# Kernel optimization log

Measured on AMD Instinct MI355X. Metric: run time of the kernel, lower is better.

Reference implementation:

```python
import jax, jax.numpy as jnp
import numpy as np

CATS = [1000, 1000, 2000]
NDS = len(CATS)
TOT = sum(CATS)          # total_cats = 4000
N = TOT + NDS            # 4003 source (label) nodes
U = 2048                 # num_unify_class
NFEAT = 256
F = 256                  # nfeat_out
OUT_FEAT = 512           # output_feat_dim
ADJ_FEAT = 256           # adj_feat_dim
SINKHORN_ITERS = 20


def setup_inputs() -> dict:
    key = jax.random.key(0)
    ks = jax.random.split(key, 16)

    def rn(k, shape, s):
        return jax.random.normal(k, shape, dtype=jnp.float32) * s

    return {
        "datasets_node_features": jax.random.normal(ks[0], (TOT, NFEAT), dtype=jnp.float32),
        "unlable_node_features": rn(ks[1], (NDS, NFEAT), 0.02),  # trunc_normal_(std=0.02)
        "adj_matrix": jax.random.uniform(ks[2], (N, U), dtype=jnp.float32),  # torch.rand init
        "W_before": rn(ks[3], (NFEAT, F), 0.05), "b_before": jnp.zeros((F,), jnp.float32),
        "gc1_W": rn(ks[4], (F, F), 0.05), "gc1_b": jnp.zeros((F,), jnp.float32),
        "gc2_W": rn(ks[5], (F, F), 0.05), "gc2_b": jnp.zeros((F,), jnp.float32),
        "gc3_W": rn(ks[6], (F, F), 0.05), "gc3_b": jnp.zeros((F,), jnp.float32),
        "W1": rn(ks[7], (F, OUT_FEAT), 0.05), "b1": jnp.zeros((OUT_FEAT,), jnp.float32),
        "W2": rn(ks[8], (OUT_FEAT, ADJ_FEAT), 0.05), "b2": jnp.zeros((ADJ_FEAT,), jnp.float32),
    }


def _log_optimal_transport(scores, iters):
    # log-space Sinkhorn with uniform marginals 1/(m+n), then rescale by (m+n)
    m, n = scores.shape
    norm = -jnp.log(jnp.asarray(m + n, scores.dtype))
    log_mu = jnp.full((m,), norm, scores.dtype)
    log_nu = jnp.full((n,), norm, scores.dtype)

    def body(carry, _):
        u, v = carry
        u = log_mu - jax.nn.logsumexp(scores + v[None, :], axis=1)
        v = log_nu - jax.nn.logsumexp(scores + u[:, None], axis=0)
        return (u, v), None

    (u, v), _ = jax.lax.scan(body, (jnp.zeros_like(log_mu), jnp.zeros_like(log_nu)),
                             None, length=iters)
    return scores + u[:, None] + v[None, :] - norm


def reference(datasets_node_features, unlable_node_features, adj_matrix,
              W_before, b_before, gc1_W, gc1_b, gc2_W, gc2_b, gc3_W, gc3_b,
              W1, b1, W2, b2):
    # node features: dataset class nodes + per-dataset 'unlabeled' nodes -> [N, NFEAT]
    feats = jnp.concatenate([datasets_node_features, unlable_node_features], axis=0)
    x = jax.nn.relu(feats @ W_before + b_before)  # [N, F]

    # learnable adjacency normalized via differentiable Sinkhorn OT  [N, U]
    A = jnp.exp(_log_optimal_transport(adj_matrix, SINKHORN_ITERS))

    # bipartite message passing: full graph adj has zero diagonal blocks,
    # so spmm(adj, h) splits into A @ h_u (into label nodes) and A.T @ h_n (into unify nodes).
    hn = x                 # [N, F] label-node features
    hu = A.T @ x           # [U, F] initial unify-node features via aggregation

    def gcn(hn, hu, W, b):
        # GraphConvolution: spmm(adj, h @ W) + b ; GCN wrapper: tanh(out + h)
        new_n = jnp.tanh(A @ (hu @ W) + b + hn)
        new_u = jnp.tanh(A.T @ (hn @ W) + b + hu)
        return new_n, new_u

    hn, hu = gcn(hn, hu, gc1_W, gc1_b)
    hn, hu = gcn(hn, hu, gc2_W, gc2_b)
    hn, hu = gcn(hn, hu, gc3_W, gc3_b)

    # output head on unify nodes: linear1 -> relu -> linear2  [U, ADJ_FEAT]
    out = jax.nn.relu(hu @ W1 + b1) @ W2 + b2
    return out
```

## Files before the change

kernel.cpp:

```cpp
#include <hip/hip_runtime.h>
#include <hip/hip_fp16.h>
#include <math.h>

#define NN 4003
#define UU 2048
#define KP 4032
#define N4P 4004
#define NORMC (-8.7079796f)

using bf16x8 = __attribute__((ext_vector_type(8))) short;
using f32x4  = __attribute__((ext_vector_type(4))) float;

#define GLL16(g, l) __builtin_amdgcn_global_load_lds( \
    (const __attribute__((address_space(1))) unsigned*)(g), \
    (__attribute__((address_space(3))) unsigned*)(l), 16, 0, 0)

__device__ __forceinline__ ushort f2bf(float x) {
    unsigned u = __builtin_bit_cast(unsigned, x);
    u += 0x7fff + ((u >> 16) & 1);
    return (ushort)(u >> 16);
}
__device__ __forceinline__ float bf2f(ushort h) {
    unsigned u = ((unsigned)h) << 16;
    return __builtin_bit_cast(float, u);
}
__device__ __forceinline__ void bfsplit(float x, ushort& hi, ushort& lo) {
    hi = f2bf(x);
    lo = f2bf(x - bf2f(hi));
}
__device__ __forceinline__ float h2f(ushort h) {
    return __half2float(__ushort_as_half(h));
}

__global__ void concat_bf(const float* __restrict__ a, const float* __restrict__ b,
                          ushort* __restrict__ fh, ushort* __restrict__ fl) {
    int i = blockIdx.x * 256 + threadIdx.x;
    const int tot4 = NN * 256 / 4;
    if (i >= tot4) return;
    float4 v = (i < 256000) ? ((const float4*)a)[i] : ((const float4*)b)[i - 256000];
    ushort4 hv, lv;
    bfsplit(v.x, hv.x, lv.x); bfsplit(v.y, hv.y, lv.y);
    bfsplit(v.z, hv.z, lv.z); bfsplit(v.w, hv.w, lv.w);
    *(ushort4*)(fh + ((size_t)i << 2)) = hv;
    *(ushort4*)(fl + ((size_t)i << 2)) = lv;
}

__global__ void convW(const float* __restrict__ W, ushort* __restrict__ Th,
                      ushort* __restrict__ Tl, int K, int Nw) {
    __shared__ float tile[32][33];
    int bx = blockIdx.x, by = blockIdx.y;
    int tx = threadIdx.x;
    for (int r = threadIdx.y; r < 32; r += 8)
        tile[r][tx] = W[(size_t)(by * 32 + r) * Nw + bx * 32 + tx];
    __syncthreads();
    for (int r = threadIdx.y; r < 32; r += 8) {
        int n = bx * 32 + r, k = by * 32 + tx;
        ushort hi, lo; bfsplit(tile[tx][r], hi, lo);
        Th[(size_t)n * K + k] = hi;
        Tl[(size_t)n * K + k] = lo;
    }
}

__global__ void conv_both(const float* __restrict__ in, ushort* __restrict__ Sh,
                          ushort* __restrict__ STh) {
    __shared__ float tile[32][33];
    int x = blockIdx.x * 32 + threadIdx.x;
    int y0 = blockIdx.y * 32;
    for (int r = threadIdx.y; r < 32; r += 8) {
        int y = y0 + r;
        float vv = (y < NN) ? in[(size_t)y * UU + x] : 0.0f;
        tile[r][threadIdx.x] = vv;
        if (y < NN)
            Sh[(size_t)y * UU + x] = __half_as_ushort(__float2half(vv));
    }
    __syncthreads();
    int oc = y0 + threadIdx.x;
    for (int r = threadIdx.y; r < 32; r += 8) {
        int orow = blockIdx.x * 32 + r;
        STh[(size_t)orow * KP + oc] = __half_as_ushort(__float2half(tile[threadIdx.x][r]));
    }
}

__global__ void init_uext(float* __restrict__ u_ext) {
    int i = threadIdx.x;
    if (i < KP - NN) u_ext[NN + i] = -1e30f;
}

__global__ __launch_bounds__(256) void lse2h(const ushort* __restrict__ Sh, int lda,
                                             const float* __restrict__ addv,
                                             float* __restrict__ outv, int C, int R) {
    int r0 = blockIdx.x * 2, r1 = r0 + 1;
    bool has1 = (r1 < R);
    const ushort* rowa = Sh + (size_t)r0 * lda;
    const ushort* rowb = Sh + (size_t)(has1 ? r1 : r0) * lda;
    const float4* a4 = (const float4*)addv;
    float m0 = -INFINITY, s0 = 0.0f, m1 = -INFINITY, s1 = 0.0f;
    int C4 = C >> 2;
    for (int j = threadIdx.x; j < C4; j += 256) {
        float4 av = a4[j];
        ushort4 pa = *(const ushort4*)(rowa + (j << 2));
        ushort4 pb = *(const ushort4*)(rowb + (j << 2));
        float a0 = h2f(pa.x) + av.x, a1 = h2f(pa.y) + av.y;
        float a2 = h2f(pa.z) + av.z, a3 = h2f(pa.w) + av.w;
        float b0 = h2f(pb.x) + av.x, b1 = h2f(pb.y) + av.y;
        float b2 = h2f(pb.z) + av.z, b3 = h2f(pb.w) + av.w;
        float mxa = fmaxf(fmaxf(a0, a1), fmaxf(a2, a3));
        float nm0 = fmaxf(m0, mxa);
        s0 = s0 * __expf(m0 - nm0) + __expf(a0 - nm0) + __expf(a1 - nm0)
                                   + __expf(a2 - nm0) + __expf(a3 - nm0);
        m0 = nm0;
        float mxb = fmaxf(fmaxf(b0, b1), fmaxf(b2, b3));
        float nm1 = fmaxf(m1, mxb);
        s1 = s1 * __expf(m1 - nm1) + __expf(b0 - nm1) + __expf(b1 - nm1)
                                   + __expf(b2 - nm1) + __expf(b3 - nm1);
        m1 = nm1;
    }
    int rem = C & 3;
    if ((int)threadIdx.x < rem) {
        int j = (C4 << 2) + threadIdx.x;
        float av = addv[j];
        float xa = h2f(rowa[j]) + av;
        float nm0 = fmaxf(m0, xa);
        s0 = s0 * __expf(m0 - nm0) + __expf(xa - nm0);
        m0 = nm0;
        float xb = h2f(rowb[j]) + av;
        float nm1 = fmaxf(m1, xb);
        s1 = s1 * __expf(m1 - nm1) + __expf(xb - nm1);
        m1 = nm1;
    }
    #pragma unroll
    for (int off = 1; off < 64; off <<= 1) {
        float om = __shfl_xor(m0, off, 64), os = __shfl_xor(s0, off, 64);
        float nm = fmaxf(m0, om);
        s0 = s0 * __expf(m0 - nm) + os * __expf(om - nm);
        m0 = nm;
        om = __shfl_xor(m1, off, 64); os = __shfl_xor(s1, off, 64);
        nm = fmaxf(m1, om);
        s1 = s1 * __expf(m1 - nm) + os * __expf(om - nm);
        m1 = nm;
    }
    __shared__ float sm[8], ss[8];
    int w = threadIdx.x >> 6;
    if ((threadIdx.x & 63) == 0) { sm[w] = m0; ss[w] = s0; sm[4 + w] = m1; ss[4 + w] = s1; }
    __syncthreads();
    if (threadIdx.x < 2) {
        int b = threadIdx.x * 4;
        float m = sm[b], s = ss[b];
        #pragma unroll
        for (int i = 1; i < 4; ++i) {
            float om = sm[b + i], os = ss[b + i];
            float nm = fmaxf(m, om);
            s = s * __expf(m - nm) + os * __expf(om - nm);
            m = nm;
        }
        int r = r0 + threadIdx.x;
        if (threadIdx.x == 0 || has1) outv[r] = NORMC - (m + __logf(s));
    }
}

__device__ __forceinline__ void exp_row8h(const ushort* __restrict__ Sh,
        const float* __restrict__ rowadd, const float* __restrict__ coladd,
        int lda, int M, int gm, int kbase, uint4& hiv, uint4& lov) {
    ushort h[8], l[8];
    if (gm < M) {
        float ra = rowadd[gm] - NORMC;
        const ushort* rp = Sh + (size_t)gm * lda + kbase;
        ushort4 q0 = *(const ushort4*)rp;
        ushort4 q1 = *(const ushort4*)(rp + 4);
        float4 ca = *(const float4*)(coladd + kbase);
        float4 cb = *(const float4*)(coladd + kbase + 4);
        float vv[8] = {h2f(q0.x) + ca.x, h2f(q0.y) + ca.y, h2f(q0.z) + ca.z, h2f(q0.w) + ca.w,
                       h2f(q1.x) + cb.x, h2f(q1.y) + cb.y, h2f(q1.z) + cb.z, h2f(q1.w) + cb.w};
        #pragma unroll
        for (int e = 0; e < 8; ++e) {
            float av = __expf(vv[e] + ra);
            bfsplit(av, h[e], l[e]);
        }
    } else {
        #pragma unroll
        for (int e = 0; e < 8; ++e) { h[e] = 0; l[e] = 0; }
    }
    hiv.x = (unsigned)h[0] | ((unsigned)h[1] << 16);
    hiv.y = (unsigned)h[2] | ((unsigned)h[3] << 16);
    hiv.z = (unsigned)h[4] | ((unsigned)h[5] << 16);
    hiv.w = (unsigned)h[6] | ((unsigned)h[7] << 16);
    lov.x = (unsigned)l[0] | ((unsigned)l[1] << 16);
    lov.y = (unsigned)l[2] | ((unsigned)l[3] << 16);
    lov.z = (unsigned)l[4] | ((unsigned)l[5] << 16);
    lov.w = (unsigned)l[6] | ((unsigned)l[7] << 16);
}

__global__ __launch_bounds__(512) __attribute__((amdgpu_waves_per_eu(2, 4)))
void gemm_bigN(
        const ushort* __restrict__ Sh, const float* __restrict__ rowadd,
        const float* __restrict__ coladd, int lda,
        const ushort* __restrict__ Bh, const ushort* __restrict__ Bl, int ldb,
        float* __restrict__ P, int M, int K, int Kc) {
    __shared__ __align__(16) ushort SM[2 * 64 * 64 + 2 * 256 * 64];
    ushort* As0 = SM;
    ushort* As1 = SM + 4096;
    ushort* Bs0 = SM + 8192;
    ushort* Bs1 = SM + 8192 + 16384;
    const int tid = threadIdx.x;
    const int bm = blockIdx.x << 6;
    const int lane = tid & 63;
    const int wv = tid >> 6;
    const int wr = (wv >> 2) << 5;
    const int wc = (wv & 3) << 6;
    const int kb = blockIdx.y * Kc;
    int ke = kb + Kc; if (ke > K) ke = K;
    const int arow = tid >> 3, ak8 = (tid & 7) << 3;
    const int as = ((arow << 6) + ak8) ^ ((arow & 7) << 3);
    const int brow_base = wv << 5;
    f32x4 acc[2][4] = {};
    for (int k0 = kb; k0 < ke; k0 += 64) {
        uint4 ah, al;
        exp_row8h(Sh, rowadd, coladd, lda, M, bm + arow, k0 + ak8, ah, al);
        __syncthreads();
        #pragma unroll
        for (int t = 0; t < 4; ++t) {
            int rb2 = brow_base + (t << 3);
            int row = rb2 + (lane >> 3);
            int kksrc = (((lane & 7) ^ (row & 7)) << 3);
            size_t go = (size_t)row * ldb + k0 + kksrc;
            GLL16(Bh + go, &Bs0[rb2 << 6]);
            GLL16(Bl + go, &Bs1[rb2 << 6]);
        }
        *(uint4*)&As0[as] = ah;
        *(uint4*)&As1[as] = al;
        __syncthreads();
        #pragma unroll
        for (int ks = 0; ks < 2; ++ks) {
            int kq = (ks << 5) + ((lane >> 4) << 3);
            bf16x8 fah[2], fal[2], fbh[4], fbl[4];
            #pragma unroll
            for (int f = 0; f < 2; ++f) {
                int rr = wr + (f << 4) + (lane & 15);
                int ia = ((rr << 6) + kq) ^ ((rr & 7) << 3);
                fah[f] = *(const bf16x8*)&As0[ia];
                fal[f] = *(const bf16x8*)&As1[ia];
            }
            #pragma unroll
            for (int g = 0; g < 4; ++g) {
                int cc = wc + (g << 4) + (lane & 15);
                int ib = ((cc << 6) + kq) ^ ((cc & 7) << 3);
                fbh[g] = *(const bf16x8*)&Bs0[ib];
                fbl[g] = *(const bf16x8*)&Bs1[ib];
            }
            #pragma unroll
            for (int i = 0; i < 2; ++i)
                #pragma unroll
                for (int j = 0; j < 4; ++j) {
                    acc[i][j] = __builtin_amdgcn_mfma_f32_16x16x32_bf16(fah[i], fbh[j], acc[i][j], 0, 0, 0);
                    acc[i][j] = __builtin_amdgcn_mfma_f32_16x16x32_bf16(fah[i], fbl[j], acc[i][j], 0, 0, 0);
                    acc[i][j] = __builtin_amdgcn_mfma_f32_16x16x32_bf16(fal[i], fbh[j], acc[i][j], 0, 0, 0);
                }
        }
    }
    __syncthreads();
    float* LF = (float*)SM;
    #pragma unroll
    for (int i = 0; i < 2; ++i) {
        int row0 = wr + (i << 4) + ((lane >> 4) << 2);
        #pragma unroll
        for (int j = 0; j < 4; ++j) {
            int col = wc + (j << 4) + (lane & 15);
            #pragma unroll
            for (int r = 0; r < 4; ++r)
                LF[(row0 + r) * 256 + col] = acc[i][j][r];
        }
    }
    __syncthreads();
    float* Pp = P + (size_t)blockIdx.y * ((size_t)M * 256);
    #pragma unroll
    for (int it = 0; it < 8; ++it) {
        int idx = tid + (it << 9);
        int row = idx >> 6, c4 = (idx & 63) << 2;
        if (bm + row < M)
            *(float4*)(Pp + (size_t)(bm + row) * 256 + c4) = *(const float4*)&LF[row * 256 + c4];
    }
}

__global__ __launch_bounds__(256) __attribute__((amdgpu_waves_per_eu(4, 8)))
void gemm_ks(
        const ushort* __restrict__ Ah, const ushort* __restrict__ Al, int lda,
        const ushort* __restrict__ Bh, const ushort* __restrict__ Bl, int ldb, int Nb,
        float* __restrict__ P, int M, int Nplane, int K, int Kc) {
    __shared__ __align__(16) ushort SM[4 * 64 * 64];
    ushort* As0 = SM;
    ushort* As1 = SM + 4096;
    ushort* Bs0 = SM + 8192;
    ushort* Bs1 = SM + 12288;
    const int tid = threadIdx.x;
    const int bm = blockIdx.y << 6, bn = blockIdx.x << 6;
    const int lane = tid & 63;
    const int wv = tid >> 6;
    const int wm = (wv >> 1) << 5, wn = (wv & 1) << 5;
    const int kb = blockIdx.z * Kc;
    int ke = kb + Kc; if (ke > K) ke = K;
    const int rb = wv << 4;
    f32x4 acc[2][2] = {};
    for (int k0 = kb; k0 < ke; k0 += 64) {
        __syncthreads();
        #pragma unroll
        for (int t = 0; t < 2; ++t) {
            int rb2 = rb + (t << 3);
            int row = rb2 + (lane >> 3);
            int kksrc = (((lane & 7) ^ (row & 7)) << 3);
            int ga = bm + row; ga = (ga < M) ? ga : (M - 1);
            int gb = bn + row; gb = (gb < Nb) ? gb : (Nb - 1);
            size_t goa = (size_t)ga * lda + k0 + kksrc;
            size_t gob = (size_t)gb * ldb + k0 + kksrc;
            GLL16(Ah + goa, &As0[rb2 << 6]);
            GLL16(Al + goa, &As1[rb2 << 6]);
            GLL16(Bh + gob, &Bs0[rb2 << 6]);
            GLL16(Bl + gob, &Bs1[rb2 << 6]);
        }
        __syncthreads();
        #pragma unroll
        for (int ks = 0; ks < 2; ++ks) {
            int kbq = (ks << 5) + ((lane >> 4) << 3);
            bf16x8 fah[2], fal[2], fbh[2], fbl[2];
            #pragma unroll
            for (int f = 0; f < 2; ++f) {
                int rr = wm + (f << 4) + (lane & 15);
                int ia = ((rr << 6) + kbq) ^ ((rr & 7) << 3);
                fah[f] = *(const bf16x8*)&As0[ia];
                fal[f] = *(const bf16x8*)&As1[ia];
                int cc = wn + (f << 4) + (lane & 15);
                int ib = ((cc << 6) + kbq) ^ ((cc & 7) << 3);
                fbh[f] = *(const bf16x8*)&Bs0[ib];
                fbl[f] = *(const bf16x8*)&Bs1[ib];
            }
            #pragma unroll
            for (int i = 0; i < 2; ++i)
                #pragma unroll
                for (int j = 0; j < 2; ++j) {
                    acc[i][j] = __builtin_amdgcn_mfma_f32_16x16x32_bf16(fah[i], fbh[j], acc[i][j], 0, 0, 0);
                    acc[i][j] = __builtin_amdgcn_mfma_f32_16x16x32_bf16(fah[i], fbl[j], acc[i][j], 0, 0, 0);
                    acc[i][j] = __builtin_amdgcn_mfma_f32_16x16x32_bf16(fal[i], fbh[j], acc[i][j], 0, 0, 0);
                }
        }
    }
    __syncthreads();
    float* LF = (float*)SM;
    #pragma unroll
    for (int i = 0; i < 2; ++i) {
        int row0 = wm + (i << 4) + ((lane >> 4) << 2);
        #pragma unroll
        for (int j = 0; j < 2; ++j) {
            int col = wn + (j << 4) + (lane & 15);
            #pragma unroll
            for (int r = 0; r < 4; ++r)
                LF[(row0 + r) * 64 + col] = acc[i][j][r];
        }
    }
    __syncthreads();
    float* Pp = P + (size_t)blockIdx.z * ((size_t)M * Nplane);
    #pragma unroll
    for (int it = 0; it < 4; ++it) {
        int idx = tid + (it << 8);
        int row = idx >> 4, c4 = (idx & 15) << 2;
        if (bm + row < M && bn + c4 < Nplane)
            *(float4*)(Pp + (size_t)(bm + row) * Nplane + bn + c4) = *(const float4*)&LF[row * 64 + c4];
    }
}

template<int ACT, int BIAS, int RES, int OUTK>
__global__ __launch_bounds__(256) void reduce_ks(
        const float* __restrict__ P, int zg,
        const float* __restrict__ bias,
        const ushort* __restrict__ Rh, const ushort* __restrict__ Rl,
        float* __restrict__ Cf, ushort* __restrict__ Ch, ushort* __restrict__ Cl,
        int M, int N4, int ldo) {
    int t = blockIdx.x * 256 + threadIdx.x;
    int n4w = N4 >> 2;
    int tot = M * n4w;
    if (t >= tot) return;
    int m = t / n4w;
    int n = (t - m * n4w) << 2;
    size_t pstr = (size_t)M * N4;
    const float* base = P + (size_t)m * N4 + n;
    float4 a = *(const float4*)base;
    for (int z = 1; z < zg; ++z) {
        float4 b = *(const float4*)(base + (size_t)z * pstr);
        a.x += b.x; a.y += b.y; a.z += b.z; a.w += b.w;
    }
    if (BIAS == 1) {
        float4 bv = *(const float4*)(bias + n);
        a.x += bv.x; a.y += bv.y; a.z += bv.z; a.w += bv.w;
    }
    if (BIAS == 2) {
        float s = bias[m];
        a.x += s; a.y += s; a.z += s; a.w += s;
    }
    if (RES) {
        size_t ro = (size_t)m * ldo + n;
        ushort4 rh = *(const ushort4*)(Rh + ro);
        ushort4 rl = *(const ushort4*)(Rl + ro);
        a.x += bf2f(rh.x) + bf2f(rl.x); a.y += bf2f(rh.y) + bf2f(rl.y);
        a.z += bf2f(rh.z) + bf2f(rl.z); a.w += bf2f(rh.w) + bf2f(rl.w);
    }
    if (ACT == 1) {
        a.x = fmaxf(a.x, 0.f); a.y = fmaxf(a.y, 0.f);
        a.z = fmaxf(a.z, 0.f); a.w = fmaxf(a.w, 0.f);
    }
    if (ACT == 2) {
        a.x = tanhf(a.x); a.y = tanhf(a.y); a.z = tanhf(a.z); a.w = tanhf(a.w);
    }
    size_t co = (size_t)m * ldo + n;
    if (OUTK == 0) {
        *(float4*)(Cf + co) = a;
    } else {
        ushort4 hv, lv;
        bfsplit(a.x, hv.x, lv.x); bfsplit(a.y, hv.y, lv.y);
        bfsplit(a.z, hv.z, lv.z); bfsplit(a.w, hv.w, lv.w);
        *(ushort4*)(Ch + co) = hv;
        *(ushort4*)(Cl + co) = lv;
    }
}

static inline int rgrid(int M, int N4) { return (M * (N4 >> 2) + 255) / 256; }

extern "C" void kernel_launch(void* const* d_in, const int* in_sizes, int n_in,
                              void* d_out, int out_size, void* d_ws, size_t ws_size,
                              hipStream_t stream) {
    const float* dsf = (const float*)d_in[0];
    const float* unl = (const float*)d_in[1];
    const float* S   = (const float*)d_in[2];
    const float* Wb  = (const float*)d_in[3];
    const float* bb  = (const float*)d_in[4];
    const float* gcW[3] = {(const float*)d_in[5], (const float*)d_in[7], (const float*)d_in[9]};
    const float* gcb[3] = {(const float*)d_in[6], (const float*)d_in[8], (const float*)d_in[10]};
    const float* W1 = (const float*)d_in[11];
    const float* b1 = (const float*)d_in[12];
    const float* W2 = (const float*)d_in[13];
    const float* b2 = (const float*)d_in[14];
    float* out = (float*)d_out;

    char* p = (char*)d_ws;
    ushort* Shm = (ushort*)p; p += (size_t)NN * UU * 2;
    ushort* STh = (ushort*)p; p += (size_t)UU * KP * 2;
    float* P    = (float*)p;  p += (size_t)8 * NN * 256 * 4;
    ushort* fh = (ushort*)p; ushort* fl = fh + (size_t)NN * 256; p += (size_t)NN * 256 * 4;
    ushort* xh = (ushort*)p; ushort* xl = xh + (size_t)NN * 256; p += (size_t)NN * 256 * 4;
    ushort* xTh = (ushort*)p; ushort* xTl = xTh + (size_t)256 * KP; p += (size_t)256 * KP * 4;
    ushort* huh = (ushort*)p; ushort* hul = huh + (size_t)UU * 256; p += (size_t)UU * 256 * 4;
    ushort* tuTh = (ushort*)p; ushort* tuTl = tuTh + (size_t)256 * UU; p += (size_t)256 * UU * 4;
    ushort* tnTh = (ushort*)p; ushort* tnTl = tnTh + (size_t)256 * KP; p += (size_t)256 * KP * 4;
    float* u_ext = (float*)p; p += KP * 4;
    float* v     = (float*)p; p += UU * 4;
    ushort* WbTh = (ushort*)p; ushort* WbTl = WbTh + 256 * 256; p += 256 * 256 * 4;
    ushort* gWh[3]; ushort* gWl[3];
    for (int l = 0; l < 3; ++l) { gWh[l] = (ushort*)p; gWl[l] = gWh[l] + 256 * 256; p += 256 * 256 * 4; }
    ushort* W1Th = (ushort*)p; ushort* W1Tl = W1Th + 512 * 256; p += 512 * 256 * 4;
    ushort* W2Th = (ushort*)p; ushort* W2Tl = W2Th + 256 * 512; p += 256 * 512 * 4;
    ushort* h1h = xh; ushort* h1l = h1h + (size_t)UU * 512;
    (void)ws_size;

    concat_bf<<<dim3(1001), dim3(256), 0, stream>>>(dsf, unl, fh, fl);
    convW<<<dim3(8, 8),  dim3(32, 8), 0, stream>>>(Wb, WbTh, WbTl, 256, 256);
    for (int l = 0; l < 3; ++l)
        convW<<<dim3(8, 8), dim3(32, 8), 0, stream>>>(gcW[l], gWh[l], gWl[l], 256, 256);
    convW<<<dim3(16, 8), dim3(32, 8), 0, stream>>>(W1, W1Th, W1Tl, 256, 512);
    convW<<<dim3(8, 16), dim3(32, 8), 0, stream>>>(W2, W2Th, W2Tl, 512, 256);
    init_uext<<<dim3(1), dim3(64), 0, stream>>>(u_ext);
    conv_both<<<dim3(64, 126), dim3(32, 8), 0, stream>>>(S, Shm, STh);
    hipMemsetAsync(v, 0, UU * sizeof(float), stream);

    gemm_ks<<<dim3(4, 63, 4), 256, 0, stream>>>(
        fh, fl, 256, WbTh, WbTl, 256, 256, P, NN, 256, 256, 64);
    reduce_ks<1,1,0,1><<<rgrid(NN,256), 256, 0, stream>>>(
        P, 4, bb, nullptr, nullptr, nullptr, xh, xl, NN, 256, 256);
    gemm_ks<<<dim3(63, 4, 4), 256, 0, stream>>>(
        WbTh, WbTl, 256, fh, fl, 256, NN, P, 256, N4P, 256, 64);
    reduce_ks<1,2,0,1><<<rgrid(256,N4P), 256, 0, stream>>>(
        P, 4, bb, nullptr, nullptr, nullptr, xTh, xTl, 256, N4P, KP);

    for (int it = 0; it < 20; ++it) {
        lse2h<<<dim3((NN + 1) / 2), dim3(256), 0, stream>>>(Shm, UU, v, u_ext, UU, NN);
        lse2h<<<dim3(UU / 2),       dim3(256), 0, stream>>>(STh, KP, u_ext, v, NN, UU);
    }

    gemm_bigN<<<dim3(32, 8), 512, 0, stream>>>(
        STh, v, u_ext, KP, xTh, xTl, KP, P, UU, KP, 512);
    reduce_ks<0,0,0,1><<<rgrid(UU,256), 256, 0, stream>>>(
        P, 8, nullptr, nullptr, nullptr, nullptr, huh, hul, UU, 256, 256);

    for (int l = 0; l < 3; ++l) {
        const ushort* hnh = (l == 0) ? xh : fh;
        const ushort* hnl = (l == 0) ? xl : fl;
        if (l < 2) {
            gemm_ks<<<dim3(32, 4, 4), 256, 0, stream>>>(
                gWh[l], gWl[l], 256, huh, hul, 256, UU, P, 256, UU, 256, 64);
            reduce_ks<0,0,0,1><<<rgrid(256,UU), 256, 0, stream>>>(
                P, 4, nullptr, nullptr, nullptr, nullptr, tuTh, tuTl, 256, UU, UU);
        }
        gemm_ks<<<dim3(63, 4, 4), 256, 0, stream>>>(
            gWh[l], gWl[l], 256, hnh, hnl, 256, NN, P, 256, N4P, 256, 64);
        reduce_ks<0,0,0,1><<<rgrid(256,N4P), 256, 0, stream>>>(
            P, 4, nullptr, nullptr, nullptr, nullptr, tnTh, tnTl, 256, N4P, KP);
        if (l < 2) {
            gemm_bigN<<<dim3(63, 8), 512, 0, stream>>>(
                Shm, u_ext, v, UU, tuTh, tuTl, UU, P, NN, UU, 256);
            reduce_ks<2,1,1,1><<<rgrid(NN,256), 256, 0, stream>>>(
                P, 8, gcb[l], hnh, hnl, nullptr, fh, fl, NN, 256, 256);
        }
        gemm_bigN<<<dim3(32, 8), 512, 0, stream>>>(
            STh, v, u_ext, KP, tnTh, tnTl, KP, P, UU, KP, 512);
        reduce_ks<2,1,1,1><<<rgrid(UU,256), 256, 0, stream>>>(
            P, 8, gcb[l], huh, hul, nullptr, huh, hul, UU, 256, 256);
    }

    gemm_ks<<<dim3(8, 32, 4), 256, 0, stream>>>(
        huh, hul, 256, W1Th, W1Tl, 256, 512, P, UU, 512, 256, 64);
    reduce_ks<1,1,0,1><<<rgrid(UU,512), 256, 0, stream>>>(
        P, 4, b1, nullptr, nullptr, nullptr, h1h, h1l, UU, 512, 512);
    gemm_ks<<<dim3(4, 32, 8), 256, 0, stream>>>(
        h1h, h1l, 512, W2Th, W2Tl, 512, 256, P, UU, 256, 512, 64);
    reduce_ks<0,1,0,0><<<rgrid(UU,256), 256, 0, stream>>>(
        P, 8, b2, nullptr, nullptr, out, nullptr, nullptr, UU, 256, 256);
}
```

Measured before the change: 587.5 us.

## Merge setup kernels, process four rows per Sinkhorn block, halve GEMM split-K

Several small setup launches are merged into single kernels: weight conversions go through one convW_all grid, and the u_ext/v initialisation is folded into concat_bf. The Sinkhorn logsumexp kernel now handles four rows per block instead of two, which reuses each addv load across more rows and halves the block count. The split-K factors of most GEMMs drop from 4 (or 8) to 2 (or 4, or 6), with larger K chunks, so less partial-sum traffic goes through reduce_ks. This costs some parallelism on the smaller GEMMs and adds register pressure in the LSE kernel.

```diff
diff --git a/kernel.cpp b/kernel.cpp
--- a/kernel.cpp
+++ b/kernel.cpp
@@ -33,22 +33,48 @@
 }
 
 __global__ void concat_bf(const float* __restrict__ a, const float* __restrict__ b,
-                          ushort* __restrict__ fh, ushort* __restrict__ fl) {
-    int i = blockIdx.x * 256 + threadIdx.x;
+                          ushort* __restrict__ fh, ushort* __restrict__ fl,
+                          float* __restrict__ u_ext, float* __restrict__ v) {
+    int bid = blockIdx.x;
+    if (bid >= 1001) {
+        if (bid < 1003) {
+            int t = (bid - 1001) * 256 + threadIdx.x;
+            if (t < 512) ((float4*)v)[t] = (float4){0.f, 0.f, 0.f, 0.f};
+        } else {
+            if ((int)threadIdx.x < KP - NN) u_ext[NN + threadIdx.x] = -1e30f;
+        }
+        return;
+    }
+    int i = bid * 256 + threadIdx.x;
     const int tot4 = NN * 256 / 4;
     if (i >= tot4) return;
-    float4 v = (i < 256000) ? ((const float4*)a)[i] : ((const float4*)b)[i - 256000];
+    float4 vv = (i < 256000) ? ((const float4*)a)[i] : ((const float4*)b)[i - 256000];
     ushort4 hv, lv;
-    bfsplit(v.x, hv.x, lv.x); bfsplit(v.y, hv.y, lv.y);
-    bfsplit(v.z, hv.z, lv.z); bfsplit(v.w, hv.w, lv.w);
+    bfsplit(vv.x, hv.x, lv.x); bfsplit(vv.y, hv.y, lv.y);
+    bfsplit(vv.z, hv.z, lv.z); bfsplit(vv.w, hv.w, lv.w);
     *(ushort4*)(fh + ((size_t)i << 2)) = hv;
     *(ushort4*)(fl + ((size_t)i << 2)) = lv;
 }
 
-__global__ void convW(const float* __restrict__ W, ushort* __restrict__ Th,
-                      ushort* __restrict__ Tl, int K, int Nw) {
+__global__ void convW_all(
+        const float* __restrict__ Wa, const float* __restrict__ Wb_,
+        const float* __restrict__ Wc, const float* __restrict__ Wd,
+        const float* __restrict__ We, const float* __restrict__ Wf,
+        ushort* T0h, ushort* T0l, ushort* T1h, ushort* T1l,
+        ushort* T2h, ushort* T2l, ushort* T3h, ushort* T3l,
+        ushort* T4h, ushort* T4l, ushort* T5h, ushort* T5l) {
     __shared__ float tile[32][33];
+    const float* W; ushort* Th; ushort* Tl; int K, Nw;
+    switch (blockIdx.z) {
+        case 0:  W = Wa;  Th = T0h; Tl = T0l; K = 256; Nw = 256; break;
+        case 1:  W = Wb_; Th = T1h; Tl = T1l; K = 256; Nw = 256; break;
+        case 2:  W = Wc;  Th = T2h; Tl = T2l; K = 256; Nw = 256; break;
+        case 3:  W = Wd;  Th = T3h; Tl = T3l; K = 256; Nw = 256; break;
+        case 4:  W = We;  Th = T4h; Tl = T4l; K = 256; Nw = 512; break;
+        default: W = Wf;  Th = T5h; Tl = T5l; K = 512; Nw = 256; break;
+    }
     int bx = blockIdx.x, by = blockIdx.y;
+    if (bx * 32 >= Nw || by * 32 >= K) return;
     int tx = threadIdx.x;
     for (int r = threadIdx.y; r < 32; r += 8)
         tile[r][tx] = W[(size_t)(by * 32 + r) * Nw + bx * 32 + tx];
@@ -81,80 +107,77 @@
     }
 }
 
-__global__ void init_uext(float* __restrict__ u_ext) {
-    int i = threadIdx.x;
-    if (i < KP - NN) u_ext[NN + i] = -1e30f;
-}
-
-__global__ __launch_bounds__(256) void lse2h(const ushort* __restrict__ Sh, int lda,
+__device__ __forceinline__ void wave_lse_reduce(float& m, float& s) {
+    #pragma unroll
+    for (int off = 1; off < 64; off <<= 1) {
+        float om = __shfl_xor(m, off, 64), os = __shfl_xor(s, off, 64);
+        float nm = fmaxf(m, om);
+        s = s * __expf(m - nm) + os * __expf(om - nm);
+        m = nm;
+    }
+}
+
+__global__ __launch_bounds__(256) void lse4h(const ushort* __restrict__ Sh, int lda,
                                              const float* __restrict__ addv,
                                              float* __restrict__ outv, int C, int R) {
-    int r0 = blockIdx.x * 2, r1 = r0 + 1;
-    bool has1 = (r1 < R);
-    const ushort* rowa = Sh + (size_t)r0 * lda;
-    const ushort* rowb = Sh + (size_t)(has1 ? r1 : r0) * lda;
-    const float4* a4 = (const float4*)addv;
-    float m0 = -INFINITY, s0 = 0.0f, m1 = -INFINITY, s1 = 0.0f;
+    int r0 = blockIdx.x * 4;
+    const ushort* rp[4];
+    #pragma unroll
+    for (int q = 0; q < 4; ++q) {
+        int r = r0 + q; if (r >= R) r = R - 1;
+        rp[q] = Sh + (size_t)r * lda;
+    }
+    float m[4], s[4];
+    #pragma unroll
+    for (int q = 0; q < 4; ++q) { m[q] = -INFINITY; s[q] = 0.0f; }
     int C4 = C >> 2;
     for (int j = threadIdx.x; j < C4; j += 256) {
-        float4 av = a4[j];
-        ushort4 pa = *(const ushort4*)(rowa + (j << 2));
-        ushort4 pb = *(const ushort4*)(rowb + (j << 2));
-        float a0 = h2f(pa.x) + av.x, a1 = h2f(pa.y) + av.y;
-        float a2 = h2f(pa.z) + av.z, a3 = h2f(pa.w) + av.w;
-        float b0 = h2f(pb.x) + av.x, b1 = h2f(pb.y) + av.y;
-        float b2 = h2f(pb.z) + av.z, b3 = h2f(pb.w) + av.w;
-        float mxa = fmaxf(fmaxf(a0, a1), fmaxf(a2, a3));
-        float nm0 = fmaxf(m0, mxa);
-        s0 = s0 * __expf(m0 - nm0) + __expf(a0 - nm0) + __expf(a1 - nm0)
-                                   + __expf(a2 - nm0) + __expf(a3 - nm0);
-        m0 = nm0;
-        float mxb = fmaxf(fmaxf(b0, b1), fmaxf(b2, b3));
-        float nm1 = fmaxf(m1, mxb);
-        s1 = s1 * __expf(m1 - nm1) + __expf(b0 - nm1) + __expf(b1 - nm1)
-                                   + __expf(b2 - nm1) + __expf(b3 - nm1);
-        m1 = nm1;
+        float4 av = ((const float4*)addv)[j];
+        #pragma unroll
+        for (int q = 0; q < 4; ++q) {
+            ushort4 pa = *(const ushort4*)(rp[q] + (j << 2));
+            float x0 = h2f(pa.x) + av.x, x1 = h2f(pa.y) + av.y;
+            float x2 = h2f(pa.z) + av.z, x3 = h2f(pa.w) + av.w;
+            float mx = fmaxf(fmaxf(x0, x1), fmaxf(x2, x3));
+            float nm = fmaxf(m[q], mx);
+            s[q] = s[q] * __expf(m[q] - nm) + __expf(x0 - nm) + __expf(x1 - nm)
+                                            + __expf(x2 - nm) + __expf(x3 - nm);
+            m[q] = nm;
+        }
     }
     int rem = C & 3;
     if ((int)threadIdx.x < rem) {
         int j = (C4 << 2) + threadIdx.x;
         float av = addv[j];
-        float xa = h2f(rowa[j]) + av;
-        float nm0 = fmaxf(m0, xa);
-        s0 = s0 * __expf(m0 - nm0) + __expf(xa - nm0);
-        m0 = nm0;
-        float xb = h2f(rowb[j]) + av;
-        float nm1 = fmaxf(m1, xb);
-        s1 = s1 * __expf(m1 - nm1) + __expf(xb - nm1);
-        m1 = nm1;
-    }
-    #pragma unroll
-    for (int off = 1; off < 64; off <<= 1) {
-        float om = __shfl_xor(m0, off, 64), os = __shfl_xor(s0, off, 64);
-        float nm = fmaxf(m0, om);
-        s0 = s0 * __expf(m0 - nm) + os * __expf(om - nm);
-        m0 = nm;
-        om = __shfl_xor(m1, off, 64); os = __shfl_xor(s1, off, 64);
-        nm = fmaxf(m1, om);
-        s1 = s1 * __expf(m1 - nm) + os * __expf(om - nm);
-        m1 = nm;
-    }
-    __shared__ float sm[8], ss[8];
+        #pragma unroll
+        for (int q = 0; q < 4; ++q) {
+            float x = h2f(rp[q][j]) + av;
+            float nm = fmaxf(m[q], x);
+            s[q] = s[q] * __expf(m[q] - nm) + __expf(x - nm);
+            m[q] = nm;
+        }
+    }
+    #pragma unroll
+    for (int q = 0; q < 4; ++q) wave_lse_reduce(m[q], s[q]);
+    __shared__ float sm[4][4], ss[4][4];
     int w = threadIdx.x >> 6;
-    if ((threadIdx.x & 63) == 0) { sm[w] = m0; ss[w] = s0; sm[4 + w] = m1; ss[4 + w] = s1; }
-    __syncthreads();
-    if (threadIdx.x < 2) {
-        int b = threadIdx.x * 4;
-        float m = sm[b], s = ss[b];
+    if ((threadIdx.x & 63) == 0) {
+        #pragma unroll
+        for (int q = 0; q < 4; ++q) { sm[w][q] = m[q]; ss[w][q] = s[q]; }
+    }
+    __syncthreads();
+    if (threadIdx.x < 4) {
+        int q = threadIdx.x;
+        float mm = sm[0][q], sa = ss[0][q];
         #pragma unroll
         for (int i = 1; i < 4; ++i) {
-            float om = sm[b + i], os = ss[b + i];
-            float nm = fmaxf(m, om);
-            s = s * __expf(m - nm) + os * __expf(om - nm);
-            m = nm;
-        }
-        int r = r0 + threadIdx.x;
-        if (threadIdx.x == 0 || has1) outv[r] = NORMC - (m + __logf(s));
+            float om = sm[i][q], os = ss[i][q];
+            float nm = fmaxf(mm, om);
+            sa = sa * __expf(mm - nm) + os * __expf(om - nm);
+            mm = nm;
+        }
+        int r = r0 + q;
+        if (r < R) outv[r] = NORMC - (mm + __logf(sa));
     }
 }
 
@@ -458,28 +481,25 @@
     ushort* h1h = xh; ushort* h1l = h1h + (size_t)UU * 512;
     (void)ws_size;
 
-    concat_bf<<<dim3(1001), dim3(256), 0, stream>>>(dsf, unl, fh, fl);
-    convW<<<dim3(8, 8),  dim3(32, 8), 0, stream>>>(Wb, WbTh, WbTl, 256, 256);
-    for (int l = 0; l < 3; ++l)
-        convW<<<dim3(8, 8), dim3(32, 8), 0, stream>>>(gcW[l], gWh[l], gWl[l], 256, 256);
-    convW<<<dim3(16, 8), dim3(32, 8), 0, stream>>>(W1, W1Th, W1Tl, 256, 512);
-    convW<<<dim3(8, 16), dim3(32, 8), 0, stream>>>(W2, W2Th, W2Tl, 512, 256);
-    init_uext<<<dim3(1), dim3(64), 0, stream>>>(u_ext);
+    concat_bf<<<dim3(1004), dim3(256), 0, stream>>>(dsf, unl, fh, fl, u_ext, v);
+    convW_all<<<dim3(16, 16, 6), dim3(32, 8), 0, stream>>>(
+        Wb, gcW[0], gcW[1], gcW[2], W1, W2,
+        WbTh, WbTl, gWh[0], gWl[0], gWh[1], gWl[1], gWh[2], gWl[2],
+        W1Th, W1Tl, W2Th, W2Tl);
     conv_both<<<dim3(64, 126), dim3(32, 8), 0, stream>>>(S, Shm, STh);
-    hipMemsetAsync(v, 0, UU * sizeof(float), stream);
-
-    gemm_ks<<<dim3(4, 63, 4), 256, 0, stream>>>(
-        fh, fl, 256, WbTh, WbTl, 256, 256, P, NN, 256, 256, 64);
+
+    gemm_ks<<<dim3(4, 63, 2), 256, 0, stream>>>(
+        fh, fl, 256, WbTh, WbTl, 256, 256, P, NN, 256, 256, 128);
     reduce_ks<1,1,0,1><<<rgrid(NN,256), 256, 0, stream>>>(
-        P, 4, bb, nullptr, nullptr, nullptr, xh, xl, NN, 256, 256);
-    gemm_ks<<<dim3(63, 4, 4), 256, 0, stream>>>(
-        WbTh, WbTl, 256, fh, fl, 256, NN, P, 256, N4P, 256, 64);
+        P, 2, bb, nullptr, nullptr, nullptr, xh, xl, NN, 256, 256);
+    gemm_ks<<<dim3(63, 4, 2), 256, 0, stream>>>(
+        WbTh, WbTl, 256, fh, fl, 256, NN, P, 256, N4P, 256, 128);
     reduce_ks<1,2,0,1><<<rgrid(256,N4P), 256, 0, stream>>>(
-        P, 4, bb, nullptr, nullptr, nullptr, xTh, xTl, 256, N4P, KP);
+        P, 2, bb, nullptr, nullptr, nullptr, xTh, xTl, 256, N4P, KP);
 
     for (int it = 0; it < 20; ++it) {
-        lse2h<<<dim3((NN + 1) / 2), dim3(256), 0, stream>>>(Shm, UU, v, u_ext, UU, NN);
-        lse2h<<<dim3(UU / 2),       dim3(256), 0, stream>>>(STh, KP, u_ext, v, NN, UU);
+        lse4h<<<dim3((NN + 3) / 4), dim3(256), 0, stream>>>(Shm, UU, v, u_ext, UU, NN);
+        lse4h<<<dim3(UU / 4),       dim3(256), 0, stream>>>(STh, KP, u_ext, v, NN, UU);
     }
 
     gemm_bigN<<<dim3(32, 8), 512, 0, stream>>>(
@@ -491,20 +511,20 @@
         const ushort* hnh = (l == 0) ? xh : fh;
         const ushort* hnl = (l == 0) ? xl : fl;
         if (l < 2) {
-            gemm_ks<<<dim3(32, 4, 4), 256, 0, stream>>>(
-                gWh[l], gWl[l], 256, huh, hul, 256, UU, P, 256, UU, 256, 64);
+            gemm_ks<<<dim3(32, 4, 2), 256, 0, stream>>>(
+                gWh[l], gWl[l], 256, huh, hul, 256, UU, P, 256, UU, 256, 128);
             reduce_ks<0,0,0,1><<<rgrid(256,UU), 256, 0, stream>>>(
-                P, 4, nullptr, nullptr, nullptr, nullptr, tuTh, tuTl, 256, UU, UU);
-        }
-        gemm_ks<<<dim3(63, 4, 4), 256, 0, stream>>>(
-            gWh[l], gWl[l], 256, hnh, hnl, 256, NN, P, 256, N4P, 256, 64);
+                P, 2, nullptr, nullptr, nullptr, nullptr, tuTh, tuTl, 256, UU, UU);
+        }
+        gemm_ks<<<dim3(63, 4, 2), 256, 0, stream>>>(
+            gWh[l], gWl[l], 256, hnh, hnl, 256, NN, P, 256, N4P, 256, 128);
         reduce_ks<0,0,0,1><<<rgrid(256,N4P), 256, 0, stream>>>(
-            P, 4, nullptr, nullptr, nullptr, nullptr, tnTh, tnTl, 256, N4P, KP);
+            P, 2, nullptr, nullptr, nullptr, nullptr, tnTh, tnTl, 256, N4P, KP);
         if (l < 2) {
-            gemm_bigN<<<dim3(63, 8), 512, 0, stream>>>(
-                Shm, u_ext, v, UU, tuTh, tuTl, UU, P, NN, UU, 256);
+            gemm_bigN<<<dim3(63, 6), 512, 0, stream>>>(
+                Shm, u_ext, v, UU, tuTh, tuTl, UU, P, NN, UU, 384);
             reduce_ks<2,1,1,1><<<rgrid(NN,256), 256, 0, stream>>>(
-                P, 8, gcb[l], hnh, hnl, nullptr, fh, fl, NN, 256, 256);
+                P, 6, gcb[l], hnh, hnl, nullptr, fh, fl, NN, 256, 256);
         }
         gemm_bigN<<<dim3(32, 8), 512, 0, stream>>>(
             STh, v, u_ext, KP, tnTh, tnTl, KP, P, UU, KP, 512);
@@ -512,12 +532,12 @@
             P, 8, gcb[l], huh, hul, nullptr, huh, hul, UU, 256, 256);
     }
 
-    gemm_ks<<<dim3(8, 32, 4), 256, 0, stream>>>(
-        huh, hul, 256, W1Th, W1Tl, 256, 512, P, UU, 512, 256, 64);
+    gemm_ks<<<dim3(8, 32, 2), 256, 0, stream>>>(
+        huh, hul, 256, W1Th, W1Tl, 256, 512, P, UU, 512, 256, 128);
     reduce_ks<1,1,0,1><<<rgrid(UU,512), 256, 0, stream>>>(
-        P, 4, b1, nullptr, nullptr, nullptr, h1h, h1l, UU, 512, 512);
-    gemm_ks<<<dim3(4, 32, 8), 256, 0, stream>>>(
-        h1h, h1l, 512, W2Th, W2Tl, 512, 256, P, UU, 256, 512, 64);
+        P, 2, b1, nullptr, nullptr, nullptr, h1h, h1l, UU, 512, 512);
+    gemm_ks<<<dim3(4, 32, 4), 256, 0, stream>>>(
+        h1h, h1l, 512, W2Th, W2Tl, 512, 256, P, UU, 256, 512, 128);
     reduce_ks<0,1,0,0><<<rgrid(UU,256), 256, 0, stream>>>(
-        P, 8, b2, nullptr, nullptr, out, nullptr, nullptr, UU, 256, 256);
-}
+        P, 4, b2, nullptr, nullptr, out, nullptr, nullptr, UU, 256, 256);
+}
```

New measurement: 560.2 us. 1.05x faster.
